# Kernel tuning notes

Hardware: AMD Instinct MI355X
Metric: run time of the kernel (lower is better)

Reference implementation:

```python
import jax, jax.numpy as jnp
import numpy as np

HEADS = 16
DIM_HEAD = 64
NUM_W = 4  # num_adaptive_weights
SCALE = DIM_HEAD ** -0.5


def setup_inputs() -> dict:
    key = jax.random.key(0)
    k0, k1, k2, k3 = jax.random.split(key, 4)
    b, n, dim = 2, 2048, 1024
    dim_inner = HEADS * DIM_HEAD  # 1024
    x = jax.random.normal(k0, (b, n, dim), jnp.float32)
    # Linear weights stored as (in, out); torch Linear(in,out,bias=False) computes x @ W.T
    Wqkv = jax.random.normal(k1, (dim, dim_inner * 3 * NUM_W), jnp.float32) * (dim ** -0.5)
    Wg = jax.random.normal(k2, (dim, NUM_W), jnp.float32) * (dim ** -0.5)
    Wout = jax.random.normal(k3, (dim_inner, dim * NUM_W), jnp.float32) * (dim_inner ** -0.5)
    mask = jnp.ones((b, n), dtype=bool)
    return {"x": x, "Wqkv": Wqkv, "Wg": Wg, "Wout": Wout, "mask": mask}


def reference(x, Wqkv, Wg, Wout, mask):
    b, n, dim = x.shape
    # to_qkv: packed last dim order is (qkv, h, d, w) per Rearrange 'b n (qkv h d w) -> qkv b h n d w'
    qkv = (x @ Wqkv).reshape(b, n, 3, HEADS, DIM_HEAD, NUM_W)
    qkv = jnp.transpose(qkv, (2, 0, 3, 1, 4, 5))  # [3, b, h, n, d, w]
    # adaptive gates: softmax over the w adaptive weights
    gates = jax.nn.softmax(x @ Wg, axis=-1)  # [b, n, w]
    # gated sum over adaptive-weight axis
    qkv = jnp.einsum('qbhndw,bnw->qbhnd', qkv, gates)
    q, k, v = qkv[0] * SCALE, qkv[1], qkv[2]
    sim = jnp.einsum('bhid,bhjd->bhij', q, k)  # [b, h, n, n]
    sim = jnp.where(mask[:, None, None, :], sim, jnp.finfo(sim.dtype).min)
    attn = jax.nn.softmax(sim, axis=-1)
    out = jnp.einsum('bhij,bhjd->bhid', attn, v)  # [b, h, n, d]
    out = out.transpose(0, 2, 1, 3).reshape(b, n, HEADS * DIM_HEAD)  # 'b h n d -> b n (h d)'
    out = (out @ Wout).reshape(b, n, dim, NUM_W)  # 'b n (d w) -> b n d w'
    # gated sum over w for the output projection
    return jnp.einsum('bndw,bnw->bnd', out, gates)
```

## Files before the change

### kernel.cpp

```cpp
#include <hip/hip_runtime.h>
#include <hip/hip_bf16.h>

#define M_TOT 4096
#define DIM_  1024
#define KP    4096
#define NC1   3072
#define NC2   1024

typedef unsigned short u16;
typedef unsigned int u32;
typedef unsigned long long u64;
typedef short bf16x8 __attribute__((ext_vector_type(8)));
typedef float f32x4 __attribute__((ext_vector_type(4)));

#define QSCALE 0.18033688011112042f
#define EXPOFF 20.0f

static __device__ __forceinline__ u16 f2bf(float f) {
    union { float f; u32 u; } v; v.f = f;
    u32 u = v.u;
    u += 0x7fffu + ((u >> 16) & 1u);
    return (u16)(u >> 16);
}
static __device__ __forceinline__ float bf2f(u16 h) {
    union { u32 u; float f; } v; v.u = ((u32)h) << 16; return v.f;
}

static __device__ __forceinline__ void gld_lds16(const u16* g, u16* l) {
    __builtin_amdgcn_global_load_lds(
        (__attribute__((address_space(1))) void*)(u64)g,
        (__attribute__((address_space(3))) void*)(u32)(u64)l,
        16, 0, 0);
}

#define SWZ_SCOL(lane) ((((lane) & 7) ^ (((lane) >> 3) & 7)) * 8)

#define RAW_BARRIER()   asm volatile("s_barrier" ::: "memory")
#define WAIT_VM0()      asm volatile("s_waitcnt vmcnt(0)" ::: "memory")
#define WAIT_LGKM0()    asm volatile("s_waitcnt lgkmcnt(0)" ::: "memory")

__global__ __launch_bounds__(256) void gates_expand_kernel(const float* __restrict__ x,
                                                           const float* __restrict__ Wg,
                                                           float* __restrict__ gates,
                                                           u16* __restrict__ outA) {
    const int wid = threadIdx.x >> 6, lane = threadIdx.x & 63;
    const int m = blockIdx.x * 4 + wid;
    const float* xr = x + (size_t)m * DIM_;
    float a0 = 0.f, a1 = 0.f, a2 = 0.f, a3 = 0.f;
    for (int i = 0; i < DIM_ / 64; ++i) {
        int k = i * 64 + lane;
        float xv = xr[k];
        float4 wg = ((const float4*)Wg)[k];
        a0 += xv * wg.x; a1 += xv * wg.y; a2 += xv * wg.z; a3 += xv * wg.w;
    }
    for (int s = 1; s < 64; s <<= 1) {
        a0 += __shfl_xor(a0, s); a1 += __shfl_xor(a1, s);
        a2 += __shfl_xor(a2, s); a3 += __shfl_xor(a3, s);
    }
    float mx = fmaxf(fmaxf(a0, a1), fmaxf(a2, a3));
    float e0 = __expf(a0 - mx), e1 = __expf(a1 - mx), e2 = __expf(a2 - mx), e3 = __expf(a3 - mx);
    float inv = 1.0f / (e0 + e1 + e2 + e3);
    float g0 = e0 * inv, g1 = e1 * inv, g2 = e2 * inv, g3 = e3 * inv;
    if (lane == 0) ((float4*)gates)[m] = make_float4(g0, g1, g2, g3);
    ushort4* out4 = (ushort4*)outA;
    for (int i = 0; i < DIM_ / 64; ++i) {
        int k = i * 64 + lane;
        float val = xr[k];
        ushort4 o;
        o.x = f2bf(val * g0); o.y = f2bf(val * g1); o.z = f2bf(val * g2); o.w = f2bf(val * g3);
        out4[(size_t)m * 1024 + k] = o;
    }
}

__global__ __launch_bounds__(256) void bprep_kernel(const float* __restrict__ src,
                                                    u16* __restrict__ dst,
                                                    int R, int Cg) {
    __shared__ u16 lds[64 * 68];
    const int t = threadIdx.x;
    const int cg0 = blockIdx.x * 16, k0 = blockIdx.y * 64;
    const float4* s4 = (const float4*)src;
    for (int i = 0; i < 4; ++i) {
        int f = i * 256 + t;
        int kl = f >> 4, f4 = f & 15;
        float4 v = s4[(size_t)(k0 + kl) * Cg + cg0 + f4];
        ushort4 o; o.x = f2bf(v.x); o.y = f2bf(v.y); o.z = f2bf(v.z); o.w = f2bf(v.w);
        *(ushort4*)&lds[kl * 68 + f4 * 4] = o;
    }
    __syncthreads();
    ushort4* d4 = (ushort4*)dst;
    for (int i = 0; i < 4; ++i) {
        int j = i * 256 + t;
        int cgl = j >> 6, kl = j & 63;
        d4[(size_t)(cg0 + cgl) * R + k0 + kl] = *(ushort4*)&lds[kl * 68 + cgl * 4];
    }
}

__global__ __launch_bounds__(256) void gemm1_kernel(const u16* __restrict__ A,
                                                    const u16* __restrict__ Bm,
                                                    u16* __restrict__ qbuf,
                                                    u16* __restrict__ kbuf,
                                                    u16* __restrict__ vbuf) {
    __shared__ u16 lA[128 * 64];
    __shared__ u16 lB[128 * 64];
    const int t = threadIdx.x;
    const int lane = t & 63, wid = t >> 6;
    const int wm = wid >> 1, wn = wid & 1;
    const int l15 = lane & 15, quad = lane >> 4;
    const int sx = l15 & 7;
    const int n0 = blockIdx.x * 128, m0 = blockIdx.y * 128;
    const int srow = lane >> 3, scol = SWZ_SCOL(lane);
    const u16* gA = A + (size_t)(m0 + wid * 32 + srow) * KP + scol;
    const u16* gB = Bm + (size_t)(n0 + wid * 32 + srow) * KP + scol;
    u16* lAw = &lA[wid * 2048];
    u16* lBw = &lB[wid * 2048];
    f32x4 acc[4][4] = {};
    for (int k0 = 0; k0 < KP; k0 += 64) {
        for (int i = 0; i < 4; ++i)
            gld_lds16(gA + (size_t)i * 8 * KP + k0, lAw + i * 512);
        for (int i = 0; i < 4; ++i)
            gld_lds16(gB + (size_t)i * 8 * KP + k0, lBw + i * 512);
        __syncthreads();
        for (int ks = 0; ks < 2; ++ks) {
            const int co = ((ks * 4 + quad) ^ sx) * 8;
            bf16x8 af[4], bfr[4];
            for (int mt = 0; mt < 4; ++mt)
                af[mt] = *(const bf16x8*)&lA[(wm * 64 + mt * 16 + l15) * 64 + co];
            for (int nt = 0; nt < 4; ++nt)
                bfr[nt] = *(const bf16x8*)&lB[(wn * 64 + nt * 16 + l15) * 64 + co];
            for (int mt = 0; mt < 4; ++mt)
                for (int nt = 0; nt < 4; ++nt)
                    acc[mt][nt] = __builtin_amdgcn_mfma_f32_16x16x32_bf16(af[mt], bfr[nt], acc[mt][nt], 0, 0, 0);
        }
        __syncthreads();
    }
    const int qkv = n0 >> 10;
    const int base_hd = n0 & 1023;
    for (int mt = 0; mt < 4; ++mt) {
        int mrow = m0 + wm * 64 + mt * 16 + quad * 4;
        int b = mrow >> 11, n = mrow & 2047;
        int bh0 = b * 16;
        for (int nt = 0; nt < 4; ++nt) {
            int hd = base_hd + wn * 64 + nt * 16 + l15;
            int h = hd >> 6, d = hd & 63;
            int bh = bh0 + h;
            if (qkv == 0) {
                for (int r = 0; r < 4; ++r)
                    qbuf[((size_t)bh * 2048 + n + r) * 64 + d] = f2bf(acc[mt][nt][r] * QSCALE);
            } else if (qkv == 1) {
                for (int r = 0; r < 4; ++r)
                    kbuf[((size_t)bh * 2048 + n + r) * 64 + d] = f2bf(acc[mt][nt][r]);
            } else {
                ushort4 o;
                o.x = f2bf(acc[mt][nt][0]); o.y = f2bf(acc[mt][nt][1]);
                o.z = f2bf(acc[mt][nt][2]); o.w = f2bf(acc[mt][nt][3]);
                *(ushort4*)&vbuf[((size_t)bh * 64 + d) * 2048 + n] = o;
            }
        }
    }
}

__global__ __launch_bounds__(256) void gemm2_kernel(const u16* __restrict__ A,
                                                    const u16* __restrict__ Bm,
                                                    float* __restrict__ outf) {
    __shared__ u16 lA[2][128 * 64];
    __shared__ u16 lB[2][64 * 64];
    const int t = threadIdx.x;
    const int lane = t & 63, wid = t >> 6;
    const int wm = wid >> 1, wn = wid & 1;
    const int l15 = lane & 15, quad = lane >> 4;
    const int sx = l15 & 7;
    const int n0 = blockIdx.x * 64, m0 = blockIdx.y * 128;
    const int srow = lane >> 3, scol = SWZ_SCOL(lane);
    const u16* gA = A + (size_t)(m0 + wid * 32 + srow) * KP + scol;
    const u16* gB = Bm + (size_t)(n0 + wid * 16 + srow) * KP + scol;
    for (int i = 0; i < 4; ++i)
        gld_lds16(gA + (size_t)i * 8 * KP, &lA[0][(wid * 32 + i * 8) * 64]);
    for (int i = 0; i < 2; ++i)
        gld_lds16(gB + (size_t)i * 8 * KP, &lB[0][(wid * 16 + i * 8) * 64]);
    f32x4 acc[4][2] = {};
    for (int it = 0; it < 64; ++it) {
        const int cur = it & 1;
        WAIT_VM0();
        RAW_BARRIER();
        if (it + 1 < 64) {
            const int k0 = (it + 1) * 64, nb = cur ^ 1;
            for (int i = 0; i < 4; ++i)
                gld_lds16(gA + (size_t)i * 8 * KP + k0, &lA[nb][(wid * 32 + i * 8) * 64]);
            for (int i = 0; i < 2; ++i)
                gld_lds16(gB + (size_t)i * 8 * KP + k0, &lB[nb][(wid * 16 + i * 8) * 64]);
        }
        for (int ks = 0; ks < 2; ++ks) {
            const int co = ((ks * 4 + quad) ^ sx) * 8;
            bf16x8 af[4], bfr[2];
            for (int mt = 0; mt < 4; ++mt)
                af[mt] = *(const bf16x8*)&lA[cur][(wm * 64 + mt * 16 + l15) * 64 + co];
            for (int nt = 0; nt < 2; ++nt)
                bfr[nt] = *(const bf16x8*)&lB[cur][(wn * 32 + nt * 16 + l15) * 64 + co];
            for (int mt = 0; mt < 4; ++mt)
                for (int nt = 0; nt < 2; ++nt)
                    acc[mt][nt] = __builtin_amdgcn_mfma_f32_16x16x32_bf16(af[mt], bfr[nt], acc[mt][nt], 0, 0, 0);
        }
    }
    for (int mt = 0; mt < 4; ++mt) {
        int mrow = m0 + wm * 64 + mt * 16 + quad * 4;
        for (int nt = 0; nt < 2; ++nt) {
            int col = n0 + wn * 32 + nt * 16 + l15;
            for (int r = 0; r < 4; ++r)
                outf[(size_t)(mrow + r) * NC2 + col] = acc[mt][nt][r];
        }
    }
}

__global__ __launch_bounds__(256) void attn_kernel(const u16* __restrict__ qbuf,
                                                   const u16* __restrict__ kbuf,
                                                   const u16* __restrict__ vbuf,
                                                   const float* __restrict__ gates,
                                                   u16* __restrict__ outA) {
    __shared__ u16 lK[2][64 * 64];
    __shared__ u16 lV[2][64 * 64];
    __shared__ u16 lP[4][2 * 16 * 72];
    const int t = threadIdx.x, lane = t & 63, wq = t >> 6;
    const int l15 = lane & 15, quad = lane >> 4;
    const int sx7 = l15 & 7;
    const int bh = blockIdx.y, q0 = blockIdx.x * 128;
    const u16* Q = qbuf + (size_t)bh * 2048 * 64;
    const u16* K = kbuf + (size_t)bh * 2048 * 64;
    const u16* V = vbuf + (size_t)bh * 64 * 2048;
    bf16x8 qf[2][2];
    for (int mt = 0; mt < 2; ++mt)
        for (int ks = 0; ks < 2; ++ks)
            qf[mt][ks] = *(const bf16x8*)&Q[(size_t)(q0 + wq * 32 + mt * 16 + l15) * 64 + ks * 32 + quad * 8];
    f32x4 Oa[2][4] = {};
    float lacc[2] = {0.f, 0.f};
    const int krow = lane >> 3, kcol = SWZ_SCOL(lane);
    const u16* gK = K + (size_t)(wq * 16 + krow) * 64 + kcol;
    const u16* gV = V + (size_t)(wq * 16 + krow) * 2048 + kcol;
    u16* lPw = lP[wq];
    gld_lds16(gK, &lK[0][(wq * 16) * 64]);
    gld_lds16(gK + (size_t)8 * 64, &lK[0][(wq * 16 + 8) * 64]);
    gld_lds16(gV, &lV[0][(wq * 16) * 64]);
    gld_lds16(gV + (size_t)8 * 2048, &lV[0][(wq * 16 + 8) * 64]);
    for (int kt = 0; kt < 32; ++kt) {
        const int cur = kt & 1;
        WAIT_VM0();
        RAW_BARRIER();
        if (kt + 1 < 32) {
            const int nxt = (kt + 1) * 64, nb = cur ^ 1;
            gld_lds16(gK + (size_t)nxt * 64, &lK[nb][(wq * 16) * 64]);
            gld_lds16(gK + (size_t)(nxt + 8) * 64, &lK[nb][(wq * 16 + 8) * 64]);
            gld_lds16(gV + nxt, &lV[nb][(wq * 16) * 64]);
            gld_lds16(gV + nxt + (size_t)8 * 2048, &lV[nb][(wq * 16 + 8) * 64]);
        }
        f32x4 S[2][4] = {};
        for (int ks = 0; ks < 2; ++ks) {
            const int co = ((ks * 4 + quad) ^ sx7) * 8;
            for (int nt = 0; nt < 4; ++nt) {
                bf16x8 kf = *(const bf16x8*)&lK[cur][(nt * 16 + l15) * 64 + co];
                S[0][nt] = __builtin_amdgcn_mfma_f32_16x16x32_bf16(kf, qf[0][ks], S[0][nt], 0, 0, 0);
                S[1][nt] = __builtin_amdgcn_mfma_f32_16x16x32_bf16(kf, qf[1][ks], S[1][nt], 0, 0, 0);
            }
        }
        for (int mt = 0; mt < 2; ++mt) {
            u16* lPm = lPw + mt * (16 * 72);
            for (int nt = 0; nt < 4; ++nt) {
                float p0 = __builtin_amdgcn_exp2f(S[mt][nt][0] - EXPOFF);
                float p1 = __builtin_amdgcn_exp2f(S[mt][nt][1] - EXPOFF);
                float p2 = __builtin_amdgcn_exp2f(S[mt][nt][2] - EXPOFF);
                float p3 = __builtin_amdgcn_exp2f(S[mt][nt][3] - EXPOFF);
                lacc[mt] += (p0 + p1) + (p2 + p3);
                uint2 pk;
                pk.x = (u32)f2bf(p0) | ((u32)f2bf(p1) << 16);
                pk.y = (u32)f2bf(p2) | ((u32)f2bf(p3) << 16);
                *(uint2*)&lPm[l15 * 72 + nt * 16 + quad * 4] = pk;
            }
        }
        WAIT_LGKM0();
        for (int ks = 0; ks < 2; ++ks) {
            const int co = ((ks * 4 + quad) ^ sx7) * 8;
            bf16x8 p0 = *(const bf16x8*)&lPw[0 * (16 * 72) + l15 * 72 + ks * 32 + quad * 8];
            bf16x8 p1 = *(const bf16x8*)&lPw[1 * (16 * 72) + l15 * 72 + ks * 32 + quad * 8];
            for (int dt = 0; dt < 4; ++dt) {
                bf16x8 vf = *(const bf16x8*)&lV[cur][(dt * 16 + l15) * 64 + co];
                Oa[0][dt] = __builtin_amdgcn_mfma_f32_16x16x32_bf16(p0, vf, Oa[0][dt], 0, 0, 0);
                Oa[1][dt] = __builtin_amdgcn_mfma_f32_16x16x32_bf16(p1, vf, Oa[1][dt], 0, 0, 0);
            }
        }
    }
    for (int mt = 0; mt < 2; ++mt) {
        lacc[mt] += __shfl_xor(lacc[mt], 16);
        lacc[mt] += __shfl_xor(lacc[mt], 32);
    }
    const int b = bh >> 4, h = bh & 15;
    ushort4* out4 = (ushort4*)outA;
    const float4* gates4 = (const float4*)gates;
    for (int mt = 0; mt < 2; ++mt) {
        for (int r = 0; r < 4; ++r) {
            int n = q0 + wq * 32 + mt * 16 + quad * 4 + r;
            int m = b * 2048 + n;
            float invl = 1.0f / __shfl(lacc[mt], quad * 4 + r);
            float4 g = gates4[m];
            for (int dt = 0; dt < 4; ++dt) {
                float val = Oa[mt][dt][r] * invl;
                ushort4 o;
                o.x = f2bf(val * g.x); o.y = f2bf(val * g.y);
                o.z = f2bf(val * g.z); o.w = f2bf(val * g.w);
                out4[(size_t)m * 1024 + h * 64 + dt * 16 + l15] = o;
            }
        }
    }
}

extern "C" void kernel_launch(void* const* d_in, const int* in_sizes, int n_in,
                              void* d_out, int out_size, void* d_ws, size_t ws_size,
                              hipStream_t stream) {
    const float* x    = (const float*)d_in[0];
    const float* Wqkv = (const float*)d_in[1];
    const float* Wg   = (const float*)d_in[2];
    const float* Wout = (const float*)d_in[3];

    char* ws = (char*)d_ws;
    size_t off = 0;
    float* gates = (float*)(ws + off); off += (size_t)1 << 16;
    u16* Aexp = (u16*)(ws + off);      off += (size_t)M_TOT * KP * 2;
    char* regB = ws + off;             off += (size_t)NC1 * KP * 2;
    u16* B1 = (u16*)regB;
    u16* B2 = (u16*)(regB + (size_t)M_TOT * NC2 * 2);
    u16* qbuf = (u16*)(ws + off); off += (size_t)32 * 2048 * 64 * 2;
    u16* kbuf = (u16*)(ws + off); off += (size_t)32 * 2048 * 64 * 2;
    u16* vbuf = (u16*)(ws + off); off += (size_t)32 * 2048 * 64 * 2;

    hipLaunchKernelGGL(gates_expand_kernel, dim3(1024), dim3(256), 0, stream,
                       x, Wg, gates, Aexp);
    hipLaunchKernelGGL(bprep_kernel, dim3(192, 16), dim3(256), 0, stream,
                       Wqkv, B1, 1024, 3072);
    hipLaunchKernelGGL(gemm1_kernel, dim3(24, 32), dim3(256), 0, stream,
                       Aexp, B1, qbuf, kbuf, vbuf);
    hipLaunchKernelGGL(bprep_kernel, dim3(64, 16), dim3(256), 0, stream,
                       Wout, B2, 1024, 1024);
    hipLaunchKernelGGL(attn_kernel, dim3(16, 32), dim3(256), 0, stream,
                       qbuf, kbuf, vbuf, gates, Aexp);
    hipLaunchKernelGGL(gemm2_kernel, dim3(16, 32), dim3(256), 0, stream,
                       Aexp, B2, (float*)d_out);
}
```

Baseline: 367.0 us.

## Retile QKV GEMM to 256x256 blocks with 4-stage async LDS pipeline

```diff
diff --git a/kernel.cpp b/kernel.cpp
--- a/kernel.cpp
+++ b/kernel.cpp
@@ -37,6 +37,8 @@
 
 #define RAW_BARRIER()   asm volatile("s_barrier" ::: "memory")
 #define WAIT_VM0()      asm volatile("s_waitcnt vmcnt(0)" ::: "memory")
+#define WAIT_VM4()      asm volatile("s_waitcnt vmcnt(4)" ::: "memory")
+#define WAIT_VM8()      asm volatile("s_waitcnt vmcnt(8)" ::: "memory")
 #define WAIT_LGKM0()    asm volatile("s_waitcnt lgkmcnt(0)" ::: "memory")
 
 __global__ __launch_bounds__(256) void gates_expand_kernel(const float* __restrict__ x,
@@ -95,48 +97,67 @@
     }
 }
 
-__global__ __launch_bounds__(256) void gemm1_kernel(const u16* __restrict__ A,
-                                                    const u16* __restrict__ Bm,
-                                                    u16* __restrict__ qbuf,
-                                                    u16* __restrict__ kbuf,
-                                                    u16* __restrict__ vbuf) {
-    __shared__ u16 lA[128 * 64];
-    __shared__ u16 lB[128 * 64];
+__global__ __launch_bounds__(512, 2) void gemm1_kernel(const u16* __restrict__ A,
+                                                       const u16* __restrict__ Bm,
+                                                       u16* __restrict__ qbuf,
+                                                       u16* __restrict__ kbuf,
+                                                       u16* __restrict__ vbuf) {
+    __shared__ u16 lA[4][256 * 32];
+    __shared__ u16 lB[4][256 * 32];
     const int t = threadIdx.x;
     const int lane = t & 63, wid = t >> 6;
-    const int wm = wid >> 1, wn = wid & 1;
+    const int wm = wid >> 2, wn = wid & 3;
     const int l15 = lane & 15, quad = lane >> 4;
-    const int sx = l15 & 7;
-    const int n0 = blockIdx.x * 128, m0 = blockIdx.y * 128;
-    const int srow = lane >> 3, scol = SWZ_SCOL(lane);
+    const int sw = (l15 >> 1) & 3;
+    const int n0 = blockIdx.x * 256, m0 = blockIdx.y * 256;
+    const int srow = lane >> 2;
+    const int scol = (((lane & 3) ^ ((lane >> 3) & 3)) * 8);
     const u16* gA = A + (size_t)(m0 + wid * 32 + srow) * KP + scol;
     const u16* gB = Bm + (size_t)(n0 + wid * 32 + srow) * KP + scol;
-    u16* lAw = &lA[wid * 2048];
-    u16* lBw = &lB[wid * 2048];
-    f32x4 acc[4][4] = {};
-    for (int k0 = 0; k0 < KP; k0 += 64) {
-        for (int i = 0; i < 4; ++i)
-            gld_lds16(gA + (size_t)i * 8 * KP + k0, lAw + i * 512);
-        for (int i = 0; i < 4; ++i)
-            gld_lds16(gB + (size_t)i * 8 * KP + k0, lBw + i * 512);
-        __syncthreads();
-        for (int ks = 0; ks < 2; ++ks) {
-            const int co = ((ks * 4 + quad) ^ sx) * 8;
-            bf16x8 af[4], bfr[4];
-            for (int mt = 0; mt < 4; ++mt)
-                af[mt] = *(const bf16x8*)&lA[(wm * 64 + mt * 16 + l15) * 64 + co];
+    u16* lAw = &lA[0][0] + wid * 32 * 32;
+    u16* lBw = &lB[0][0] + wid * 32 * 32;
+
+#define G1_STAGE(tt) do {                                              \
+        const int _s = (tt) & 3;                                       \
+        const size_t _k = (size_t)(tt) * 32;                           \
+        gld_lds16(gA + _k,                    lAw + _s * 8192);        \
+        gld_lds16(gA + _k + (size_t)16 * KP,  lAw + _s * 8192 + 512);  \
+        gld_lds16(gB + _k,                    lBw + _s * 8192);        \
+        gld_lds16(gB + _k + (size_t)16 * KP,  lBw + _s * 8192 + 512);  \
+    } while (0)
+
+    f32x4 acc[8][4] = {};
+    G1_STAGE(0); G1_STAGE(1); G1_STAGE(2);
+    const int co = (quad ^ sw) * 8;
+    for (int kt = 0; kt < 128; ++kt) {
+        if (kt < 126)      WAIT_VM8();
+        else if (kt == 126) WAIT_VM4();
+        else               WAIT_VM0();
+        RAW_BARRIER();
+        if (kt < 125) G1_STAGE(kt + 3);
+        const u16* sA = &lA[kt & 3][0];
+        const u16* sB = &lB[kt & 3][0];
+        bf16x8 af[8], bfr[4];
+#pragma unroll
+        for (int mt = 0; mt < 8; ++mt)
+            af[mt] = *(const bf16x8*)&sA[(wm * 128 + mt * 16 + l15) * 32 + co];
+#pragma unroll
+        for (int nt = 0; nt < 4; ++nt)
+            bfr[nt] = *(const bf16x8*)&sB[(wn * 64 + nt * 16 + l15) * 32 + co];
+        __builtin_amdgcn_s_setprio(1);
+#pragma unroll
+        for (int mt = 0; mt < 8; ++mt)
+#pragma unroll
             for (int nt = 0; nt < 4; ++nt)
-                bfr[nt] = *(const bf16x8*)&lB[(wn * 64 + nt * 16 + l15) * 64 + co];
-            for (int mt = 0; mt < 4; ++mt)
-                for (int nt = 0; nt < 4; ++nt)
-                    acc[mt][nt] = __builtin_amdgcn_mfma_f32_16x16x32_bf16(af[mt], bfr[nt], acc[mt][nt], 0, 0, 0);
-        }
-        __syncthreads();
-    }
+                acc[mt][nt] = __builtin_amdgcn_mfma_f32_16x16x32_bf16(af[mt], bfr[nt], acc[mt][nt], 0, 0, 0);
+        __builtin_amdgcn_s_setprio(0);
+    }
+#undef G1_STAGE
+
     const int qkv = n0 >> 10;
     const int base_hd = n0 & 1023;
-    for (int mt = 0; mt < 4; ++mt) {
-        int mrow = m0 + wm * 64 + mt * 16 + quad * 4;
+    for (int mt = 0; mt < 8; ++mt) {
+        int mrow = m0 + wm * 128 + mt * 16 + quad * 4;
         int b = mrow >> 11, n = mrow & 2047;
         int bh0 = b * 16;
         for (int nt = 0; nt < 4; ++nt) {
@@ -333,7 +354,7 @@
                        x, Wg, gates, Aexp);
     hipLaunchKernelGGL(bprep_kernel, dim3(192, 16), dim3(256), 0, stream,
                        Wqkv, B1, 1024, 3072);
-    hipLaunchKernelGGL(gemm1_kernel, dim3(24, 32), dim3(256), 0, stream,
+    hipLaunchKernelGGL(gemm1_kernel, dim3(12, 16), dim3(512), 0, stream,
                        Aexp, B1, qbuf, kbuf, vbuf);
     hipLaunchKernelGGL(bprep_kernel, dim3(64, 16), dim3(256), 0, stream,
                        Wout, B2, 1024, 1024);
```

Result: slower. 392.5 us (+6.9%).
